# Kernel optimization log

Hardware: AMD Instinct MI355X
Metric: run time of the kernel (lower is better)

The kernel has to match this reference:

```python
import jax, jax.numpy as jnp
import numpy as np

B, NQ, NK, D, H = 4, 2048, 2048, 1024, 16
DH = D // H
SCALE = DH ** -0.5


def setup_inputs() -> dict:
    key = jax.random.key(0)
    ks = jax.random.split(key, 8)
    s = 0.02
    return {
        "x_q": jax.random.normal(ks[0], (B, NQ, D), dtype=jnp.float32),
        "x_kv": jax.random.normal(ks[1], (B, NK, D), dtype=jnp.float32),
        "Wq": jax.random.normal(ks[2], (D, D), dtype=jnp.float32) * s,
        "bq": jnp.zeros((D,), dtype=jnp.float32),
        "Wkv": jax.random.normal(ks[3], (D, 2 * D), dtype=jnp.float32) * s,
        "bkv": jnp.zeros((2 * D,), dtype=jnp.float32),
        "Wp": jax.random.normal(ks[4], (D, D), dtype=jnp.float32) * s,
        "bp": jnp.zeros((D,), dtype=jnp.float32),
    }


def reference(x_q, x_kv, Wq, bq, Wkv, bkv, Wp, bp):
    # q: [B, H, Nq, Dh]
    q = (x_q @ Wq + bq).reshape(B, NQ, H, DH).transpose(0, 2, 1, 3)
    kv = (x_kv @ Wkv + bkv).reshape(B, NK, 2, H, DH)
    k = kv[:, :, 0].transpose(0, 2, 1, 3)  # [B, H, Nk, Dh]
    v = kv[:, :, 1].transpose(0, 2, 1, 3)  # [B, H, Nk, Dh]
    attn = jnp.einsum("bhqd,bhkd->bhqk", q, k) * SCALE  # [B, H, Nq, Nk]
    attn = jax.nn.softmax(attn, axis=-1)
    out = jnp.einsum("bhqk,bhkd->bhqd", attn, v)  # [B, H, Nq, Dh]
    out = out.transpose(0, 2, 1, 3).reshape(B, NQ, D)
    return jnp.nan_to_num(x_q + out @ Wp + bp)
```

## Files before the change

kernel.cpp:

```cpp
#include <hip/hip_runtime.h>
#include <hip/hip_bf16.h>

#define B_   4
#define NQ_  2048
#define NK_  2048
#define D_   1024
#define H_   16
#define DH_  64
#define SCALE_ 0.125f

typedef __attribute__((ext_vector_type(8))) __bf16 bf16x8;
typedef __attribute__((ext_vector_type(4))) float  f32x4;

typedef const __attribute__((address_space(1))) unsigned int* gas1p;
typedef __attribute__((address_space(3))) unsigned int*       las3p;

__device__ __forceinline__ f32x4 mfma16(bf16x8 a, bf16x8 b, f32x4 c) {
  return __builtin_amdgcn_mfma_f32_16x16x32_bf16(a, b, c, 0, 0, 0);
}
__device__ __forceinline__ void gload_lds16(const void* g, void* l) {
  __builtin_amdgcn_global_load_lds((gas1p)g, (las3p)l, 16, 0, 0);
}
__device__ __forceinline__ float nn_(float x) {
  if (__builtin_isnan(x)) return 0.0f;
  if (__builtin_isinf(x)) return x > 0.f ? 3.402823466e38f : -3.402823466e38f;
  return x;
}
__device__ __forceinline__ float exp2_(float x) {
#if __has_builtin(__builtin_amdgcn_exp2f)
  return __builtin_amdgcn_exp2f(x);
#else
  return __expf(x * 0.69314718056f);
#endif
}
__device__ __forceinline__ float fmax3_(float a, float b, float c) {
  return fmaxf(fmaxf(a, b), c);
}

__global__ __launch_bounds__(256) void cvt_bf16_k(const float* __restrict__ s,
                                                  __bf16* __restrict__ d, int n) {
  int i = (blockIdx.x * blockDim.x + threadIdx.x) << 2;
  if (i >= n) return;
  float4 v = *(const float4*)(s + i);
  __bf16 o[4] __attribute__((aligned(8))) = {(__bf16)v.x, (__bf16)v.y, (__bf16)v.z, (__bf16)v.w};
  *(uint2*)(d + i) = *(uint2*)o;
}

__global__ __launch_bounds__(256) void transpose_cvt_k(const float* __restrict__ src,
                                                       __bf16* __restrict__ dst,
                                                       int K, int N, float scale) {
  __shared__ float t[32][33];
  int n0 = blockIdx.x * 32, k0 = blockIdx.y * 32;
  int x = threadIdx.x, y0 = threadIdx.y;
  for (int yy = y0; yy < 32; yy += 8)
    t[yy][x] = src[(size_t)(k0 + yy) * N + n0 + x];
  __syncthreads();
  for (int yy = y0; yy < 32; yy += 8)
    dst[(size_t)(n0 + yy) * K + k0 + x] = (__bf16)(t[x][yy] * scale);
}

template <bool OUT_BF16, bool RES>
__global__ __launch_bounds__(512, 4) void gemm3p_k(const __bf16* __restrict__ A,
                                                   const __bf16* __restrict__ Bt,
                                                   const float* __restrict__ bias, float bscale,
                                                   const float* __restrict__ res,
                                                   void* __restrict__ out,
                                                   int M, int N, int K) {
  constexpr int BM = 256, BN = 128, BK = 32;
  __shared__ __attribute__((aligned(16))) __bf16 Al[3][BM * BK];
  __shared__ __attribute__((aligned(16))) __bf16 Bl[3][BN * BK];
  const int tid = threadIdx.x, lane = tid & 63, wid = tid >> 6;
  const int wr = wid >> 1, wc = wid & 1;
  const int g = lane >> 4, lr = lane & 15;
  const int m0 = blockIdx.y * BM, n0 = blockIdx.x * BN;

  const int ca1 = tid + 512;
  const int rowA0 = tid >> 2, rowA1 = ca1 >> 2, rowB = tid >> 2;
  const __bf16* aSrc0 = A + (size_t)(m0 + rowA0) * K + (((tid & 3) ^ (rowA0 & 3)) << 3);
  const __bf16* aSrc1 = A + (size_t)(m0 + rowA1) * K + (((ca1 & 3) ^ (rowA1 & 3)) << 3);
  const __bf16* bSrc  = Bt + (size_t)(n0 + rowB) * K + (((tid & 3) ^ (rowB & 3)) << 3);
  char* aDst0 = (char*)&Al[0][0] + (tid << 4);
  char* aDst1 = (char*)&Al[0][0] + (ca1 << 4);
  char* bDst  = (char*)&Bl[0][0] + (tid << 4);

  const int swz = (lr & 3) << 4;
  int offA[4], offB[4];
#pragma unroll
  for (int m = 0; m < 4; m++) offA[m] = (wr * 64 + m * 16 + lr) * 64 + ((g * 16) ^ swz);
#pragma unroll
  for (int n = 0; n < 4; n++) offB[n] = (wc * 64 + n * 16 + lr) * 64 + ((g * 16) ^ swz);

  const f32x4 zero4 = {0.f, 0.f, 0.f, 0.f};
  f32x4 acc[4][4];
#pragma unroll
  for (int m = 0; m < 4; m++)
#pragma unroll
    for (int n = 0; n < 4; n++) acc[m][n] = zero4;

  gload_lds16(aSrc0, aDst0); gload_lds16(aSrc1, aDst1); gload_lds16(bSrc, bDst);
  gload_lds16(aSrc0 + BK, aDst0 + 16384); gload_lds16(aSrc1 + BK, aDst1 + 16384);
  gload_lds16(bSrc + BK, bDst + 8192);
  asm volatile("s_waitcnt vmcnt(3)" ::: "memory");
  __builtin_amdgcn_s_barrier();

  const int KT = K / BK;
  int cb = 0, b2 = 2;
  for (int t = 0; t < KT; ++t) {
    const char* Ab = (const char*)&Al[0][0] + cb * 16384;
    const char* Bb = (const char*)&Bl[0][0] + cb * 8192;
    bf16x8 af[4], bv[4];
#pragma unroll
    for (int m = 0; m < 4; m++) af[m] = *(const bf16x8*)(Ab + offA[m]);
#pragma unroll
    for (int n = 0; n < 4; n++) bv[n] = *(const bf16x8*)(Bb + offB[n]);
    if (t < KT - 2) {
      const int k2 = (t + 2) * BK;
      gload_lds16(aSrc0 + k2, aDst0 + b2 * 16384);
      gload_lds16(aSrc1 + k2, aDst1 + b2 * 16384);
      gload_lds16(bSrc + k2, bDst + b2 * 8192);
    }
    __builtin_amdgcn_s_setprio(1);
#pragma unroll
    for (int m = 0; m < 4; m++)
#pragma unroll
      for (int n = 0; n < 4; n++) acc[m][n] = mfma16(af[m], bv[n], acc[m][n]);
    __builtin_amdgcn_s_setprio(0);
    if (t < KT - 2)       asm volatile("s_waitcnt vmcnt(3)" ::: "memory");
    else if (t == KT - 2) asm volatile("s_waitcnt vmcnt(0)" ::: "memory");
    if (t < KT - 1) __builtin_amdgcn_s_barrier();
    cb = (cb == 2) ? 0 : cb + 1;
    b2 = (b2 == 2) ? 0 : b2 + 1;
  }

#pragma unroll
  for (int Mi = 0; Mi < 4; ++Mi) {
    int row = m0 + wr * 64 + Mi * 16 + g * 4;
#pragma unroll
    for (int Ni = 0; Ni < 4; ++Ni) {
      int col = n0 + wc * 64 + Ni * 16 + lr;
      float bvv = bias[col] * bscale;
#pragma unroll
      for (int r = 0; r < 4; ++r) {
        size_t idx = (size_t)(row + r) * N + col;
        float v = acc[Mi][Ni][r] + bvv;
        if (RES) v = nn_(v + res[idx]);
        if (OUT_BF16) ((__bf16*)out)[idx] = (__bf16)v;
        else          ((float*)out)[idx] = v;
      }
    }
  }
}

__global__ __launch_bounds__(256) void reorder_v_k(const __bf16* __restrict__ kv,
                                                   __bf16* __restrict__ vt) {
  __shared__ __attribute__((aligned(16))) __bf16 t[64][72];
  int bh = blockIdx.y, b = bh >> 4, h = bh & 15;
  int kk0 = blockIdx.x * 64;
  int tid = threadIdx.x;
#pragma unroll
  for (int i = 0; i < 2; i++) {
    int c = tid + i * 256;
    int kk = c >> 3, dc = c & 7;
    const __bf16* src = kv + (size_t)(b * NK_ + kk0 + kk) * 2048 + 1024 + h * 64 + dc * 8;
    *(float4*)&t[kk][dc * 8] = *(const float4*)src;
  }
  __syncthreads();
#pragma unroll
  for (int i = 0; i < 2; i++) {
    int c = tid + i * 256;
    int d = c >> 3, gch = c & 7;
    int s = gch ^ (d & 7);
    __bf16 tmp[8] __attribute__((aligned(16)));
#pragma unroll
    for (int j = 0; j < 8; j++) tmp[j] = t[s * 8 + j][d];
    __bf16* dst = vt + ((size_t)bh * 64 + d) * (size_t)NK_ + kk0 + gch * 8;
    *(float4*)dst = *(float4*)tmp;
  }
}

__global__ __launch_bounds__(256) void attn_k(const __bf16* __restrict__ Qg,
                                              const __bf16* __restrict__ KVg,
                                              const __bf16* __restrict__ Vt,
                                              __bf16* __restrict__ AO) {
  __shared__ __attribute__((aligned(16))) __bf16 Kt[2][64 * 64];
  __shared__ __attribute__((aligned(16))) __bf16 Vl[2][64 * 64];
  __shared__ __attribute__((aligned(16))) __bf16 Pl[4][16 * 64];
  const int tid = threadIdx.x, lane = tid & 63, wid = tid >> 6;
  const int g = lane >> 4, lr = lane & 15;
  const int bid = blockIdx.x;
  const int bh = bid & 63, b = bh >> 4, h = bh & 15;
  const int qbase = (bid >> 6) * 64 + wid * 16;

  bf16x8 qf[2];
  {
    const __bf16* qp = Qg + ((size_t)(b * NQ_ + qbase + lr)) * 1024 + h * 64 + g * 8;
    qf[0] = *(const bf16x8*)qp;
    qf[1] = *(const bf16x8*)(qp + 32);
  }

  const f32x4 zero4 = {0.f, 0.f, 0.f, 0.f};
  f32x4 po[4];
#pragma unroll
  for (int df = 0; df < 4; df++) po[df] = zero4;
  float m2 = -1e30f, l = 0.f;

  char* pw = (char*)&Pl[wid][0];
  const int pswz = (lr & 7) << 4;
  int wa[4], ra[2];
#pragma unroll
  for (int n = 0; n < 4; n++) wa[n] = lr * 128 + ((n * 32 + g * 8) ^ pswz);
#pragma unroll
  for (int ks = 0; ks < 2; ks++) ra[ks] = lr * 128 + ((ks * 64 + g * 16) ^ pswz);

  const int kk = wid * 16 + (lane >> 3);
  const int cc = lane & 7;
  const __bf16* kp0 = KVg + (size_t)b * NK_ * 2048 + h * 64 + (size_t)kk * 2048 + ((cc ^ (kk & 7)) << 3);
  const __bf16* kp1 = kp0 + 8 * 2048;
  const __bf16* vp0 = Vt + (size_t)bh * 64 * (size_t)NK_ + (size_t)kk * NK_ + (cc << 3);
  const __bf16* vp1 = vp0 + 8 * NK_;
  char* kd0 = (char*)&Kt[0][0] + wid * 2048;
  char* vd0 = (char*)&Vl[0][0] + wid * 2048;

#define STAGE_(bi)                                             \
  {                                                            \
    gload_lds16(kp0, kd0 + (bi) * 8192);                       \
    gload_lds16(kp1, kd0 + (bi) * 8192 + 1024);                \
    gload_lds16(vp0, vd0 + (bi) * 8192);                       \
    gload_lds16(vp1, vd0 + (bi) * 8192 + 1024);                \
    kp0 += 64 * 2048; kp1 += 64 * 2048; vp0 += 64; vp1 += 64;  \
  }

#define BODY_(bi)                                                                              \
  {                                                                                            \
    const char* Kb = (const char*)&Kt[bi][0];                                                  \
    const char* Vb = (const char*)&Vl[bi][0];                                                  \
    f32x4 sa[4];                                                                               \
    __builtin_amdgcn_s_setprio(1);                                                             \
    _Pragma("unroll") for (int n = 0; n < 4; n++) {                                            \
      sa[n] = zero4;                                                                           \
      int kr = n * 16 + lr;                                                                    \
      _Pragma("unroll") for (int ds = 0; ds < 2; ds++) {                                       \
        bf16x8 kf = *(const bf16x8*)(Kb + kr * 128 + ((ds * 64 + g * 16) ^ ((kr & 7) << 4)));  \
        sa[n] = mfma16(kf, qf[ds], sa[n]);                                                     \
      }                                                                                        \
    }                                                                                          \
    __builtin_amdgcn_s_setprio(0);                                                             \
    float mx = fmax3_(sa[0][0], sa[0][1], sa[0][2]);                                           \
    mx = fmax3_(mx, sa[0][3], sa[1][0]);                                                       \
    mx = fmax3_(mx, sa[1][1], sa[1][2]);                                                       \
    mx = fmax3_(mx, sa[1][3], sa[2][0]);                                                       \
    mx = fmax3_(mx, sa[2][1], sa[2][2]);                                                       \
    mx = fmax3_(mx, sa[2][3], sa[3][0]);                                                       \
    mx = fmax3_(mx, sa[3][1], sa[3][2]);                                                       \
    mx = fmaxf(mx, sa[3][3]);                                                                  \
    mx = fmaxf(mx, __shfl_xor(mx, 16));                                                        \
    mx = fmaxf(mx, __shfl_xor(mx, 32));                                                        \
    if (__any(mx > m2 + 11.0f)) {                                                              \
      float mn = fmaxf(m2, mx);                                                                \
      float alpha = exp2_(m2 - mn);                                                            \
      m2 = mn;                                                                                 \
      l *= alpha;                                                                              \
      _Pragma("unroll") for (int r = 0; r < 4; r++) {                                          \
        float ar = __shfl(alpha, g * 4 + r);                                                   \
        _Pragma("unroll") for (int df = 0; df < 4; df++) po[df][r] *= ar;                      \
      }                                                                                        \
    }                                                                                          \
    float rs = 0.f;                                                                            \
    _Pragma("unroll") for (int n = 0; n < 4; n++) {                                            \
      union { __bf16 hh[4]; uint2 u; } qd;                                                     \
      _Pragma("unroll") for (int r = 0; r < 4; r++) {                                          \
        float p = exp2_(sa[n][r] - m2);                                                        \
        rs += p;                                                                               \
        qd.hh[r] = (__bf16)p;                                                                  \
      }                                                                                        \
      *(uint2*)(pw + wa[n]) = qd.u;                                                            \
    }                                                                                          \
    rs += __shfl_xor(rs, 16);                                                                  \
    rs += __shfl_xor(rs, 32);                                                                  \
    l += rs;                                                                                   \
    bf16x8 pa[2];                                                                              \
    _Pragma("unroll") for (int ks = 0; ks < 2; ks++)                                           \
      pa[ks] = *(const bf16x8*)(pw + ra[ks]);                                                  \
    __builtin_amdgcn_s_setprio(1);                                                             \
    _Pragma("unroll") for (int df = 0; df < 4; df++) {                                         \
      int d = df * 16 + lr;                                                                    \
      _Pragma("unroll") for (int ks = 0; ks < 2; ks++) {                                       \
        bf16x8 vf = *(const bf16x8*)(Vb + d * 128 + ((ks * 64 + g * 16) ^ ((d & 7) << 4)));    \
        po[df] = mfma16(pa[ks], vf, po[df]);                                                   \
      }                                                                                        \
    }                                                                                          \
    __builtin_amdgcn_s_setprio(0);                                                             \
  }

  STAGE_(0);

#pragma unroll 1
  for (int it = 0; it < 16; ++it) {
    STAGE_(1);
    asm volatile("s_waitcnt vmcnt(4)" ::: "memory");
    asm volatile("s_barrier" ::: "memory");
    BODY_(0);
    asm volatile("s_barrier" ::: "memory");
    if (it < 15) {
      STAGE_(0);
      asm volatile("s_waitcnt vmcnt(4)" ::: "memory");
    } else {
      asm volatile("s_waitcnt vmcnt(0)" ::: "memory");
    }
    asm volatile("s_barrier" ::: "memory");
    BODY_(1);
    asm volatile("s_barrier" ::: "memory");
  }

  float inv = 1.0f / l;
#pragma unroll
  for (int r = 0; r < 4; r++) {
    float ir = __shfl(inv, g * 4 + r);
    size_t row = (size_t)(b * NQ_ + qbase + g * 4 + r);
#pragma unroll
    for (int df = 0; df < 4; df++)
      AO[row * 1024 + h * 64 + df * 16 + lr] = (__bf16)(po[df][r] * ir);
  }
#undef STAGE_
#undef BODY_
}

extern "C" void kernel_launch(void* const* d_in, const int* in_sizes, int n_in,
                              void* d_out, int out_size, void* d_ws, size_t ws_size,
                              hipStream_t stream) {
  (void)in_sizes; (void)n_in; (void)out_size; (void)ws_size;
  const float* x_q  = (const float*)d_in[0];
  const float* x_kv = (const float*)d_in[1];
  const float* Wq   = (const float*)d_in[2];
  const float* bq   = (const float*)d_in[3];
  const float* Wkv  = (const float*)d_in[4];
  const float* bkv  = (const float*)d_in[5];
  const float* Wp   = (const float*)d_in[6];
  const float* bp   = (const float*)d_in[7];

  char* w = (char*)d_ws;
  __bf16* xq_bf  = (__bf16*)w; w += (size_t)8388608 * 2;
  __bf16* xkv_bf = (__bf16*)w; w += (size_t)8388608 * 2;
  __bf16* Wq_t   = (__bf16*)w; w += (size_t)1048576 * 2;
  __bf16* Wkv_t  = (__bf16*)w; w += (size_t)2097152 * 2;
  __bf16* Wp_t   = (__bf16*)w; w += (size_t)1048576 * 2;
  __bf16* Q_bf   = (__bf16*)w; w += (size_t)8388608 * 2;
  __bf16* KV_bf  = (__bf16*)w; w += (size_t)16777216 * 2;
  __bf16* Vt     = (__bf16*)w; w += (size_t)8388608 * 2;
  __bf16* AO     = (__bf16*)w; w += (size_t)8388608 * 2;

  const float C2 = SCALE_ * 1.44269504089f;

  cvt_bf16_k<<<8192, 256, 0, stream>>>(x_q, xq_bf, 8388608);
  cvt_bf16_k<<<8192, 256, 0, stream>>>(x_kv, xkv_bf, 8388608);
  transpose_cvt_k<<<dim3(32, 32), dim3(32, 8), 0, stream>>>(Wq, Wq_t, 1024, 1024, C2);
  transpose_cvt_k<<<dim3(64, 32), dim3(32, 8), 0, stream>>>(Wkv, Wkv_t, 1024, 2048, 1.0f);
  transpose_cvt_k<<<dim3(32, 32), dim3(32, 8), 0, stream>>>(Wp, Wp_t, 1024, 1024, 1.0f);

  gemm3p_k<true, false><<<dim3(8, 32), 512, 0, stream>>>(xq_bf, Wq_t, bq, C2, nullptr, Q_bf, 8192, 1024, 1024);
  gemm3p_k<true, false><<<dim3(16, 32), 512, 0, stream>>>(xkv_bf, Wkv_t, bkv, 1.0f, nullptr, KV_bf, 8192, 2048, 1024);
  reorder_v_k<<<dim3(32, 64), 256, 0, stream>>>(KV_bf, Vt);
  attn_k<<<2048, 256, 0, stream>>>(Q_bf, KV_bf, Vt, AO);
  gemm3p_k<false, true><<<dim3(8, 32), 512, 0, stream>>>(AO, Wp_t, bp, 1.0f, x_q, d_out, 8192, 1024, 1024);
}
```

Before: 389.9 us.

## Double queries per attention wave and reorganize LDS tiles into fragment-major layout

The attention kernel now has each wave process 32 query rows (two 16-row groups) against each staged K/V tile. This halves the grid and the total K/V global-to-LDS traffic per query. Both the GEMM and attention shared-memory tiles switch from XOR-swizzled row layouts to a fragment-major layout, so each lane reads contiguous 16-byte slots at fixed offsets, and the V reorder drops its swizzle. The cost is more registers per wave for the doubled accumulators and Q fragments, which may lower occupancy, plus larger P scratch buffers.

```diff
diff --git a/kernel.cpp b/kernel.cpp
--- a/kernel.cpp
+++ b/kernel.cpp
@@ -74,21 +74,16 @@
   const int g = lane >> 4, lr = lane & 15;
   const int m0 = blockIdx.y * BM, n0 = blockIdx.x * BN;
 
-  const int ca1 = tid + 512;
-  const int rowA0 = tid >> 2, rowA1 = ca1 >> 2, rowB = tid >> 2;
-  const __bf16* aSrc0 = A + (size_t)(m0 + rowA0) * K + (((tid & 3) ^ (rowA0 & 3)) << 3);
-  const __bf16* aSrc1 = A + (size_t)(m0 + rowA1) * K + (((ca1 & 3) ^ (rowA1 & 3)) << 3);
-  const __bf16* bSrc  = Bt + (size_t)(n0 + rowB) * K + (((tid & 3) ^ (rowB & 3)) << 3);
-  char* aDst0 = (char*)&Al[0][0] + (tid << 4);
-  char* aDst1 = (char*)&Al[0][0] + (ca1 << 4);
-  char* bDst  = (char*)&Bl[0][0] + (tid << 4);
-
-  const int swz = (lr & 3) << 4;
-  int offA[4], offB[4];
-#pragma unroll
-  for (int m = 0; m < 4; m++) offA[m] = (wr * 64 + m * 16 + lr) * 64 + ((g * 16) ^ swz);
-#pragma unroll
-  for (int n = 0; n < 4; n++) offB[n] = (wc * 64 + n * 16 + lr) * 64 + ((g * 16) ^ swz);
+  const int cA0 = tid, cA1 = tid + 512, cB = tid;
+  const int rA0 = ((cA0 >> 8) << 6) + (((cA0 >> 6) & 3) << 4) + (cA0 & 15);
+  const int rA1 = ((cA1 >> 8) << 6) + (((cA1 >> 6) & 3) << 4) + (cA1 & 15);
+  const int rB  = ((cB  >> 8) << 6) + (((cB  >> 6) & 3) << 4) + (cB  & 15);
+  const __bf16* aS0 = A  + (size_t)(m0 + rA0) * K + (((cA0 >> 4) & 3) << 3);
+  const __bf16* aS1 = A  + (size_t)(m0 + rA1) * K + (((cA1 >> 4) & 3) << 3);
+  const __bf16* bS  = Bt + (size_t)(n0 + rB)  * K + (((cB  >> 4) & 3) << 3);
+  char* aD0 = (char*)&Al[0][0] + (tid << 4);
+  char* aD1 = aD0 + 8192;
+  char* bD  = (char*)&Bl[0][0] + (tid << 4);
 
   const f32x4 zero4 = {0.f, 0.f, 0.f, 0.f};
   f32x4 acc[4][4];
@@ -97,27 +92,29 @@
 #pragma unroll
     for (int n = 0; n < 4; n++) acc[m][n] = zero4;
 
-  gload_lds16(aSrc0, aDst0); gload_lds16(aSrc1, aDst1); gload_lds16(bSrc, bDst);
-  gload_lds16(aSrc0 + BK, aDst0 + 16384); gload_lds16(aSrc1 + BK, aDst1 + 16384);
-  gload_lds16(bSrc + BK, bDst + 8192);
+  gload_lds16(aS0, aD0); gload_lds16(aS1, aD1); gload_lds16(bS, bD);
+  gload_lds16(aS0 + BK, aD0 + 16384); gload_lds16(aS1 + BK, aD1 + 16384);
+  gload_lds16(bS + BK, bD + 8192);
+  aS0 += 2 * BK; aS1 += 2 * BK; bS += 2 * BK;
   asm volatile("s_waitcnt vmcnt(3)" ::: "memory");
   __builtin_amdgcn_s_barrier();
 
   const int KT = K / BK;
   int cb = 0, b2 = 2;
+  const int labase = lane << 4;
   for (int t = 0; t < KT; ++t) {
-    const char* Ab = (const char*)&Al[0][0] + cb * 16384;
-    const char* Bb = (const char*)&Bl[0][0] + cb * 8192;
+    const char* Ab = (const char*)&Al[0][0] + cb * 16384 + ((wr * 4) << 10) + labase;
+    const char* Bb = (const char*)&Bl[0][0] + cb * 8192  + ((wc * 4) << 10) + labase;
     bf16x8 af[4], bv[4];
 #pragma unroll
-    for (int m = 0; m < 4; m++) af[m] = *(const bf16x8*)(Ab + offA[m]);
-#pragma unroll
-    for (int n = 0; n < 4; n++) bv[n] = *(const bf16x8*)(Bb + offB[n]);
+    for (int m = 0; m < 4; m++) af[m] = *(const bf16x8*)(Ab + (m << 10));
+#pragma unroll
+    for (int n = 0; n < 4; n++) bv[n] = *(const bf16x8*)(Bb + (n << 10));
     if (t < KT - 2) {
-      const int k2 = (t + 2) * BK;
-      gload_lds16(aSrc0 + k2, aDst0 + b2 * 16384);
-      gload_lds16(aSrc1 + k2, aDst1 + b2 * 16384);
-      gload_lds16(bSrc + k2, bDst + b2 * 8192);
+      gload_lds16(aS0, aD0 + b2 * 16384);
+      gload_lds16(aS1, aD1 + b2 * 16384);
+      gload_lds16(bS, bD + b2 * 8192);
+      aS0 += BK; aS1 += BK; bS += BK;
     }
     __builtin_amdgcn_s_setprio(1);
 #pragma unroll
@@ -169,10 +166,9 @@
   for (int i = 0; i < 2; i++) {
     int c = tid + i * 256;
     int d = c >> 3, gch = c & 7;
-    int s = gch ^ (d & 7);
     __bf16 tmp[8] __attribute__((aligned(16)));
 #pragma unroll
-    for (int j = 0; j < 8; j++) tmp[j] = t[s * 8 + j][d];
+    for (int j = 0; j < 8; j++) tmp[j] = t[gch * 8 + j][d];
     __bf16* dst = vt + ((size_t)bh * 64 + d) * (size_t)NK_ + kk0 + gch * 8;
     *(float4*)dst = *(float4*)tmp;
   }
@@ -184,25 +180,28 @@
                                               __bf16* __restrict__ AO) {
   __shared__ __attribute__((aligned(16))) __bf16 Kt[2][64 * 64];
   __shared__ __attribute__((aligned(16))) __bf16 Vl[2][64 * 64];
-  __shared__ __attribute__((aligned(16))) __bf16 Pl[4][16 * 64];
+  __shared__ __attribute__((aligned(16))) __bf16 Pl[4][32 * 64];
   const int tid = threadIdx.x, lane = tid & 63, wid = tid >> 6;
   const int g = lane >> 4, lr = lane & 15;
   const int bid = blockIdx.x;
   const int bh = bid & 63, b = bh >> 4, h = bh & 15;
-  const int qbase = (bid >> 6) * 64 + wid * 16;
-
-  bf16x8 qf[2];
-  {
-    const __bf16* qp = Qg + ((size_t)(b * NQ_ + qbase + lr)) * 1024 + h * 64 + g * 8;
-    qf[0] = *(const bf16x8*)qp;
-    qf[1] = *(const bf16x8*)(qp + 32);
+  const int qbase = (bid >> 6) * 128 + wid * 32;
+
+  bf16x8 qf[2][2];
+#pragma unroll
+  for (int qg = 0; qg < 2; ++qg) {
+    const __bf16* qp = Qg + ((size_t)(b * NQ_ + qbase + qg * 16 + lr)) * 1024 + h * 64 + g * 8;
+    qf[qg][0] = *(const bf16x8*)qp;
+    qf[qg][1] = *(const bf16x8*)(qp + 32);
   }
 
   const f32x4 zero4 = {0.f, 0.f, 0.f, 0.f};
-  f32x4 po[4];
-#pragma unroll
-  for (int df = 0; df < 4; df++) po[df] = zero4;
-  float m2 = -1e30f, l = 0.f;
+  f32x4 po[2][4];
+#pragma unroll
+  for (int qg = 0; qg < 2; ++qg)
+#pragma unroll
+    for (int df = 0; df < 4; df++) po[qg][df] = zero4;
+  float m2[2] = {-1e30f, -1e30f}, l[2] = {0.f, 0.f};
 
   char* pw = (char*)&Pl[wid][0];
   const int pswz = (lr & 7) << 4;
@@ -212,84 +211,87 @@
 #pragma unroll
   for (int ks = 0; ks < 2; ks++) ra[ks] = lr * 128 + ((ks * 64 + g * 16) ^ pswz);
 
-  const int kk = wid * 16 + (lane >> 3);
-  const int cc = lane & 7;
-  const __bf16* kp0 = KVg + (size_t)b * NK_ * 2048 + h * 64 + (size_t)kk * 2048 + ((cc ^ (kk & 7)) << 3);
-  const __bf16* kp1 = kp0 + 8 * 2048;
-  const __bf16* vp0 = Vt + (size_t)bh * 64 * (size_t)NK_ + (size_t)kk * NK_ + (cc << 3);
-  const __bf16* vp1 = vp0 + 8 * NK_;
-  char* kd0 = (char*)&Kt[0][0] + wid * 2048;
-  char* vd0 = (char*)&Vl[0][0] + wid * 2048;
+  const int cK0 = tid, cK1 = tid + 256;
+  const int kk0r = ((cK0 >> 7) << 4) + (cK0 & 15), kk1r = ((cK1 >> 7) << 4) + (cK1 & 15);
+  const int kc0 = (((cK0 >> 6) & 1) << 5) + (((cK0 >> 4) & 3) << 3);
+  const int kc1 = (((cK1 >> 6) & 1) << 5) + (((cK1 >> 4) & 3) << 3);
+  const __bf16* kp0 = KVg + (size_t)(b * NK_ + kk0r) * 2048 + h * 64 + kc0;
+  const __bf16* kp1 = KVg + (size_t)(b * NK_ + kk1r) * 2048 + h * 64 + kc1;
+  const int vd0 = ((cK0 >> 7) << 4) + (cK0 & 15), vd1 = ((cK1 >> 7) << 4) + (cK1 & 15);
+  const __bf16* vp0 = Vt + (size_t)(bh * 64 + vd0) * NK_ + kc0;
+  const __bf16* vp1 = Vt + (size_t)(bh * 64 + vd1) * NK_ + kc1;
+  char* kD0 = (char*)&Kt[0][0] + (tid << 4);
+  char* vD0 = (char*)&Vl[0][0] + (tid << 4);
 
 #define STAGE_(bi)                                             \
   {                                                            \
-    gload_lds16(kp0, kd0 + (bi) * 8192);                       \
-    gload_lds16(kp1, kd0 + (bi) * 8192 + 1024);                \
-    gload_lds16(vp0, vd0 + (bi) * 8192);                       \
-    gload_lds16(vp1, vd0 + (bi) * 8192 + 1024);                \
+    gload_lds16(kp0, kD0 + (bi) * 8192);                       \
+    gload_lds16(kp1, kD0 + (bi) * 8192 + 4096);                \
+    gload_lds16(vp0, vD0 + (bi) * 8192);                       \
+    gload_lds16(vp1, vD0 + (bi) * 8192 + 4096);                \
     kp0 += 64 * 2048; kp1 += 64 * 2048; vp0 += 64; vp1 += 64;  \
   }
 
-#define BODY_(bi)                                                                              \
-  {                                                                                            \
-    const char* Kb = (const char*)&Kt[bi][0];                                                  \
-    const char* Vb = (const char*)&Vl[bi][0];                                                  \
-    f32x4 sa[4];                                                                               \
-    __builtin_amdgcn_s_setprio(1);                                                             \
-    _Pragma("unroll") for (int n = 0; n < 4; n++) {                                            \
-      sa[n] = zero4;                                                                           \
-      int kr = n * 16 + lr;                                                                    \
-      _Pragma("unroll") for (int ds = 0; ds < 2; ds++) {                                       \
-        bf16x8 kf = *(const bf16x8*)(Kb + kr * 128 + ((ds * 64 + g * 16) ^ ((kr & 7) << 4)));  \
-        sa[n] = mfma16(kf, qf[ds], sa[n]);                                                     \
-      }                                                                                        \
-    }                                                                                          \
-    __builtin_amdgcn_s_setprio(0);                                                             \
-    float mx = fmax3_(sa[0][0], sa[0][1], sa[0][2]);                                           \
-    mx = fmax3_(mx, sa[0][3], sa[1][0]);                                                       \
-    mx = fmax3_(mx, sa[1][1], sa[1][2]);                                                       \
-    mx = fmax3_(mx, sa[1][3], sa[2][0]);                                                       \
-    mx = fmax3_(mx, sa[2][1], sa[2][2]);                                                       \
-    mx = fmax3_(mx, sa[2][3], sa[3][0]);                                                       \
-    mx = fmax3_(mx, sa[3][1], sa[3][2]);                                                       \
-    mx = fmaxf(mx, sa[3][3]);                                                                  \
-    mx = fmaxf(mx, __shfl_xor(mx, 16));                                                        \
-    mx = fmaxf(mx, __shfl_xor(mx, 32));                                                        \
-    if (__any(mx > m2 + 11.0f)) {                                                              \
-      float mn = fmaxf(m2, mx);                                                                \
-      float alpha = exp2_(m2 - mn);                                                            \
-      m2 = mn;                                                                                 \
-      l *= alpha;                                                                              \
-      _Pragma("unroll") for (int r = 0; r < 4; r++) {                                          \
-        float ar = __shfl(alpha, g * 4 + r);                                                   \
-        _Pragma("unroll") for (int df = 0; df < 4; df++) po[df][r] *= ar;                      \
-      }                                                                                        \
-    }                                                                                          \
-    float rs = 0.f;                                                                            \
-    _Pragma("unroll") for (int n = 0; n < 4; n++) {                                            \
-      union { __bf16 hh[4]; uint2 u; } qd;                                                     \
-      _Pragma("unroll") for (int r = 0; r < 4; r++) {                                          \
-        float p = exp2_(sa[n][r] - m2);                                                        \
-        rs += p;                                                                               \
-        qd.hh[r] = (__bf16)p;                                                                  \
-      }                                                                                        \
-      *(uint2*)(pw + wa[n]) = qd.u;                                                            \
-    }                                                                                          \
-    rs += __shfl_xor(rs, 16);                                                                  \
-    rs += __shfl_xor(rs, 32);                                                                  \
-    l += rs;                                                                                   \
-    bf16x8 pa[2];                                                                              \
-    _Pragma("unroll") for (int ks = 0; ks < 2; ks++)                                           \
-      pa[ks] = *(const bf16x8*)(pw + ra[ks]);                                                  \
-    __builtin_amdgcn_s_setprio(1);                                                             \
-    _Pragma("unroll") for (int df = 0; df < 4; df++) {                                         \
-      int d = df * 16 + lr;                                                                    \
-      _Pragma("unroll") for (int ks = 0; ks < 2; ks++) {                                       \
-        bf16x8 vf = *(const bf16x8*)(Vb + d * 128 + ((ks * 64 + g * 16) ^ ((d & 7) << 4)));    \
-        po[df] = mfma16(pa[ks], vf, po[df]);                                                   \
-      }                                                                                        \
-    }                                                                                          \
-    __builtin_amdgcn_s_setprio(0);                                                             \
+#define BODY_(bi)                                                                       \
+  {                                                                                     \
+    const char* Kb = (const char*)&Kt[bi][0] + (lane << 4);                             \
+    const char* Vb = (const char*)&Vl[bi][0] + (lane << 4);                             \
+    _Pragma("unroll") for (int qg = 0; qg < 2; ++qg) {                                  \
+      f32x4 sa[4];                                                                      \
+      __builtin_amdgcn_s_setprio(1);                                                    \
+      _Pragma("unroll") for (int n = 0; n < 4; n++) {                                   \
+        sa[n] = zero4;                                                                  \
+        _Pragma("unroll") for (int ds = 0; ds < 2; ds++) {                              \
+          bf16x8 kf = *(const bf16x8*)(Kb + ((n * 2 + ds) << 10));                      \
+          sa[n] = mfma16(kf, qf[qg][ds], sa[n]);                                        \
+        }                                                                               \
+      }                                                                                 \
+      __builtin_amdgcn_s_setprio(0);                                                    \
+      float mx = fmax3_(sa[0][0], sa[0][1], sa[0][2]);                                  \
+      mx = fmax3_(mx, sa[0][3], sa[1][0]);                                              \
+      mx = fmax3_(mx, sa[1][1], sa[1][2]);                                              \
+      mx = fmax3_(mx, sa[1][3], sa[2][0]);                                              \
+      mx = fmax3_(mx, sa[2][1], sa[2][2]);                                              \
+      mx = fmax3_(mx, sa[2][3], sa[3][0]);                                              \
+      mx = fmax3_(mx, sa[3][1], sa[3][2]);                                              \
+      mx = fmaxf(mx, sa[3][3]);                                                         \
+      mx = fmaxf(mx, __shfl_xor(mx, 16));                                               \
+      mx = fmaxf(mx, __shfl_xor(mx, 32));                                               \
+      if (__any(mx > m2[qg] + 11.0f)) {                                                 \
+        float mn = fmaxf(m2[qg], mx);                                                   \
+        float alpha = exp2_(m2[qg] - mn);                                               \
+        m2[qg] = mn;                                                                    \
+        l[qg] *= alpha;                                                                 \
+        _Pragma("unroll") for (int r = 0; r < 4; r++) {                                 \
+          float ar = __shfl(alpha, g * 4 + r);                                          \
+          _Pragma("unroll") for (int df = 0; df < 4; df++) po[qg][df][r] *= ar;         \
+        }                                                                               \
+      }                                                                                 \
+      float rs = 0.f;                                                                   \
+      _Pragma("unroll") for (int n = 0; n < 4; n++) {                                   \
+        union { __bf16 hh[4]; uint2 u; } qd;                                            \
+        _Pragma("unroll") for (int r = 0; r < 4; r++) {                                 \
+          float p = exp2_(sa[n][r] - m2[qg]);                                           \
+          rs += p;                                                                      \
+          qd.hh[r] = (__bf16)p;                                                         \
+        }                                                                               \
+        *(uint2*)(pw + qg * 2048 + wa[n]) = qd.u;                                       \
+      }                                                                                 \
+      rs += __shfl_xor(rs, 16);                                                         \
+      rs += __shfl_xor(rs, 32);                                                         \
+      l[qg] += rs;                                                                      \
+      bf16x8 pa[2];                                                                     \
+      _Pragma("unroll") for (int ks = 0; ks < 2; ks++)                                  \
+        pa[ks] = *(const bf16x8*)(pw + qg * 2048 + ra[ks]);                             \
+      __builtin_amdgcn_s_setprio(1);                                                    \
+      _Pragma("unroll") for (int df = 0; df < 4; df++) {                                \
+        _Pragma("unroll") for (int ks = 0; ks < 2; ks++) {                              \
+          bf16x8 vf = *(const bf16x8*)(Vb + ((df * 2 + ks) << 10));                     \
+          po[qg][df] = mfma16(pa[ks], vf, po[qg][df]);                                  \
+        }                                                                               \
+      }                                                                                 \
+      __builtin_amdgcn_s_setprio(0);                                                    \
+    }                                                                                   \
   }
 
   STAGE_(0);
@@ -312,14 +314,17 @@
     asm volatile("s_barrier" ::: "memory");
   }
 
-  float inv = 1.0f / l;
-#pragma unroll
-  for (int r = 0; r < 4; r++) {
-    float ir = __shfl(inv, g * 4 + r);
-    size_t row = (size_t)(b * NQ_ + qbase + g * 4 + r);
-#pragma unroll
-    for (int df = 0; df < 4; df++)
-      AO[row * 1024 + h * 64 + df * 16 + lr] = (__bf16)(po[df][r] * ir);
+#pragma unroll
+  for (int qg = 0; qg < 2; ++qg) {
+    float inv = 1.0f / l[qg];
+#pragma unroll
+    for (int r = 0; r < 4; r++) {
+      float ir = __shfl(inv, g * 4 + r);
+      size_t row = (size_t)(b * NQ_ + qbase + qg * 16 + g * 4 + r);
+#pragma unroll
+      for (int df = 0; df < 4; df++)
+        AO[row * 1024 + h * 64 + df * 16 + lr] = (__bf16)(po[qg][df][r] * ir);
+    }
   }
 #undef STAGE_
 #undef BODY_
@@ -360,6 +365,6 @@
   gemm3p_k<true, false><<<dim3(8, 32), 512, 0, stream>>>(xq_bf, Wq_t, bq, C2, nullptr, Q_bf, 8192, 1024, 1024);
   gemm3p_k<true, false><<<dim3(16, 32), 512, 0, stream>>>(xkv_bf, Wkv_t, bkv, 1.0f, nullptr, KV_bf, 8192, 2048, 1024);
   reorder_v_k<<<dim3(32, 64), 256, 0, stream>>>(KV_bf, Vt);
-  attn_k<<<2048, 256, 0, stream>>>(Q_bf, KV_bf, Vt, AO);
+  attn_k<<<1024, 256, 0, stream>>>(Q_bf, KV_bf, Vt, AO);
   gemm3p_k<false, true><<<dim3(8, 32), 512, 0, stream>>>(AO, Wp_t, bp, 1.0f, x_q, d_out, 8192, 1024, 1024);
 }
```

Result: slower. 412.7 us (+5.8%).

## Remap GEMM tiles across XCDs and use a fragment-ordered LDS layout

Applied to the files above, without the earlier changes.

The GEMM grid becomes 1D and block IDs are remapped so that each of the 8 XCDs gets a contiguous range of output tiles, which is meant to improve L2 reuse. The global-to-LDS copy now writes data in MFMA fragment order, so each lane reads its operand at lane*16 plus a constant offset, with no XOR swizzle. Source pointers are also advanced incrementally instead of being recomputed each iteration. The risk is LDS bank conflicts on the direct-to-LDS writes, and the remap assumes the grid size is divisible by 8.

```diff
diff --git a/kernel.cpp b/kernel.cpp
--- a/kernel.cpp
+++ b/kernel.cpp
@@ -65,30 +65,28 @@
                                                    const float* __restrict__ bias, float bscale,
                                                    const float* __restrict__ res,
                                                    void* __restrict__ out,
-                                                   int M, int N, int K) {
+                                                   int M, int N, int K, int nX) {
   constexpr int BM = 256, BN = 128, BK = 32;
   __shared__ __attribute__((aligned(16))) __bf16 Al[3][BM * BK];
   __shared__ __attribute__((aligned(16))) __bf16 Bl[3][BN * BK];
   const int tid = threadIdx.x, lane = tid & 63, wid = tid >> 6;
   const int wr = wid >> 1, wc = wid & 1;
   const int g = lane >> 4, lr = lane & 15;
-  const int m0 = blockIdx.y * BM, n0 = blockIdx.x * BN;
-
-  const int ca1 = tid + 512;
-  const int rowA0 = tid >> 2, rowA1 = ca1 >> 2, rowB = tid >> 2;
-  const __bf16* aSrc0 = A + (size_t)(m0 + rowA0) * K + (((tid & 3) ^ (rowA0 & 3)) << 3);
-  const __bf16* aSrc1 = A + (size_t)(m0 + rowA1) * K + (((ca1 & 3) ^ (rowA1 & 3)) << 3);
-  const __bf16* bSrc  = Bt + (size_t)(n0 + rowB) * K + (((tid & 3) ^ (rowB & 3)) << 3);
-  char* aDst0 = (char*)&Al[0][0] + (tid << 4);
-  char* aDst1 = (char*)&Al[0][0] + (ca1 << 4);
-  char* bDst  = (char*)&Bl[0][0] + (tid << 4);
-
-  const int swz = (lr & 3) << 4;
-  int offA[4], offB[4];
-#pragma unroll
-  for (int m = 0; m < 4; m++) offA[m] = (wr * 64 + m * 16 + lr) * 64 + ((g * 16) ^ swz);
-#pragma unroll
-  for (int n = 0; n < 4; n++) offB[n] = (wc * 64 + n * 16 + lr) * 64 + ((g * 16) ^ swz);
+
+  const int per = gridDim.x >> 3;
+  const int wg = (blockIdx.x & 7) * per + (blockIdx.x >> 3);
+  const int m0 = (wg / nX) * BM, n0 = (wg % nX) * BN;
+
+  const int cA0 = tid, cA1 = tid + 512, cB = tid;
+  const int rA0 = ((cA0 >> 8) << 6) + (((cA0 >> 6) & 3) << 4) + (cA0 & 15);
+  const int rA1 = ((cA1 >> 8) << 6) + (((cA1 >> 6) & 3) << 4) + (cA1 & 15);
+  const int rB  = ((cB  >> 8) << 6) + (((cB  >> 6) & 3) << 4) + (cB  & 15);
+  const __bf16* aS0 = A  + (size_t)(m0 + rA0) * K + (((cA0 >> 4) & 3) << 3);
+  const __bf16* aS1 = A  + (size_t)(m0 + rA1) * K + (((cA1 >> 4) & 3) << 3);
+  const __bf16* bS  = Bt + (size_t)(n0 + rB)  * K + (((cB  >> 4) & 3) << 3);
+  char* aD0 = (char*)&Al[0][0] + (tid << 4);
+  char* aD1 = aD0 + 8192;
+  char* bD  = (char*)&Bl[0][0] + (tid << 4);
 
   const f32x4 zero4 = {0.f, 0.f, 0.f, 0.f};
   f32x4 acc[4][4];
@@ -97,27 +95,29 @@
 #pragma unroll
     for (int n = 0; n < 4; n++) acc[m][n] = zero4;
 
-  gload_lds16(aSrc0, aDst0); gload_lds16(aSrc1, aDst1); gload_lds16(bSrc, bDst);
-  gload_lds16(aSrc0 + BK, aDst0 + 16384); gload_lds16(aSrc1 + BK, aDst1 + 16384);
-  gload_lds16(bSrc + BK, bDst + 8192);
+  gload_lds16(aS0, aD0); gload_lds16(aS1, aD1); gload_lds16(bS, bD);
+  gload_lds16(aS0 + BK, aD0 + 16384); gload_lds16(aS1 + BK, aD1 + 16384);
+  gload_lds16(bS + BK, bD + 8192);
+  aS0 += 2 * BK; aS1 += 2 * BK; bS += 2 * BK;
   asm volatile("s_waitcnt vmcnt(3)" ::: "memory");
   __builtin_amdgcn_s_barrier();
 
   const int KT = K / BK;
   int cb = 0, b2 = 2;
+  const int labase = lane << 4;
   for (int t = 0; t < KT; ++t) {
-    const char* Ab = (const char*)&Al[0][0] + cb * 16384;
-    const char* Bb = (const char*)&Bl[0][0] + cb * 8192;
+    const char* Ab = (const char*)&Al[0][0] + cb * 16384 + ((wr * 4) << 10) + labase;
+    const char* Bb = (const char*)&Bl[0][0] + cb * 8192  + ((wc * 4) << 10) + labase;
     bf16x8 af[4], bv[4];
 #pragma unroll
-    for (int m = 0; m < 4; m++) af[m] = *(const bf16x8*)(Ab + offA[m]);
-#pragma unroll
-    for (int n = 0; n < 4; n++) bv[n] = *(const bf16x8*)(Bb + offB[n]);
+    for (int m = 0; m < 4; m++) af[m] = *(const bf16x8*)(Ab + (m << 10));
+#pragma unroll
+    for (int n = 0; n < 4; n++) bv[n] = *(const bf16x8*)(Bb + (n << 10));
     if (t < KT - 2) {
-      const int k2 = (t + 2) * BK;
-      gload_lds16(aSrc0 + k2, aDst0 + b2 * 16384);
-      gload_lds16(aSrc1 + k2, aDst1 + b2 * 16384);
-      gload_lds16(bSrc + k2, bDst + b2 * 8192);
+      gload_lds16(aS0, aD0 + b2 * 16384);
+      gload_lds16(aS1, aD1 + b2 * 16384);
+      gload_lds16(bS, bD + b2 * 8192);
+      aS0 += BK; aS1 += BK; bS += BK;
     }
     __builtin_amdgcn_s_setprio(1);
 #pragma unroll
@@ -357,9 +357,9 @@
   transpose_cvt_k<<<dim3(64, 32), dim3(32, 8), 0, stream>>>(Wkv, Wkv_t, 1024, 2048, 1.0f);
   transpose_cvt_k<<<dim3(32, 32), dim3(32, 8), 0, stream>>>(Wp, Wp_t, 1024, 1024, 1.0f);
 
-  gemm3p_k<true, false><<<dim3(8, 32), 512, 0, stream>>>(xq_bf, Wq_t, bq, C2, nullptr, Q_bf, 8192, 1024, 1024);
-  gemm3p_k<true, false><<<dim3(16, 32), 512, 0, stream>>>(xkv_bf, Wkv_t, bkv, 1.0f, nullptr, KV_bf, 8192, 2048, 1024);
+  gemm3p_k<true, false><<<256, 512, 0, stream>>>(xq_bf, Wq_t, bq, C2, nullptr, Q_bf, 8192, 1024, 1024, 8);
+  gemm3p_k<true, false><<<512, 512, 0, stream>>>(xkv_bf, Wkv_t, bkv, 1.0f, nullptr, KV_bf, 8192, 2048, 1024, 16);
   reorder_v_k<<<dim3(32, 64), 256, 0, stream>>>(KV_bf, Vt);
   attn_k<<<2048, 256, 0, stream>>>(Q_bf, KV_bf, Vt, AO);
-  gemm3p_k<false, true><<<dim3(8, 32), 512, 0, stream>>>(AO, Wp_t, bp, 1.0f, x_q, d_out, 8192, 1024, 1024);
-}
+  gemm3p_k<false, true><<<256, 512, 0, stream>>>(AO, Wp_t, bp, 1.0f, x_q, d_out, 8192, 1024, 1024, 8);
+}
```

Result: no change. 388.9 us (-0.3%).
